# Kernel optimization log

Measured on AMD Instinct MI355X. Metric: run time of the kernel, lower is better.

The kernel has to match this reference:

```python
import jax, jax.numpy as jnp
import numpy as np

OBS = 128; N_AGENT = 16; N_ACTION = 8; N_LAYER = 2; HID = 128
GE = 256; LE = 256; F1 = 512; F2 = 512


def _edges(batch_size, n):
    # all ordered pairs (i, j), i != j, within each sample; GCNConv adds self-loops
    i, j = np.meshgrid(np.arange(n), np.arange(n), indexing='ij')
    m = i != j
    src0, dst0 = i[m], j[m]                      # [n*(n-1)]
    off = (np.arange(batch_size) * n)[:, None]
    src = (src0[None, :] + off).reshape(-1)
    dst = (dst0[None, :] + off).reshape(-1)
    return jnp.asarray(src, jnp.int32), jnp.asarray(dst, jnp.int32)


def setup_inputs() -> dict:
    key = jax.random.key(0)
    ks = jax.random.split(key, 16)
    g = lambda k, shp, fan: jax.random.normal(k, shp, jnp.float32) / np.sqrt(fan)
    return {
        'obs_j': jax.random.normal(ks[0], (2048, N_AGENT, OBS), jnp.float32),
        'W_pre': g(ks[1], (OBS, HID), OBS), 'b_pre': jnp.zeros((HID,), jnp.float32),
        'W_gcn': g(ks[2], (N_LAYER, HID, HID), HID), 'b_gcn': jnp.zeros((N_LAYER, HID), jnp.float32),
        'W_post': g(ks[3], (HID, GE), HID), 'b_post': jnp.zeros((GE,), jnp.float32),
        'W_loc': g(ks[4], (OBS, LE), OBS), 'b_loc': jnp.zeros((LE,), jnp.float32),
        'W1': g(ks[5], (GE + LE, F1), GE + LE), 'b1': jnp.zeros((F1,), jnp.float32),
        'W2': g(ks[6], (F1, F2), F1), 'b2': jnp.zeros((F2,), jnp.float32),
        'W3': g(ks[7], (F2, N_ACTION), F2), 'b3': jnp.zeros((N_ACTION,), jnp.float32),
    }


def reference(obs_j, W_pre, b_pre, W_gcn, b_gcn, W_post, b_post,
              W_loc, b_loc, W1, b1, W2, b2, W3, b3):
    B, n, _ = obs_j.shape
    N = B * n
    obs = obs_j.reshape(N, OBS)
    x = jax.nn.relu(obs @ W_pre + b_pre)          # [N, HID]

    src, dst = _edges(B, n)
    # GCNConv with self-loops on a fully-connected graph: deg = n for every node,
    # edge norm = 1/sqrt(deg_i*deg_j) = 1/n for every (A+I) edge.
    inv_n = jnp.float32(1.0) / n
    for l in range(N_LAYER):
        h = x @ W_gcn[l]                          # lin (no bias inside propagate)
        agg = jax.ops.segment_sum(h[src], dst, num_segments=N)  # neighbor gather/scatter
        x = jax.nn.relu((agg + h) * inv_n + b_gcn[l])            # + self-loop msg, bias

    g = x.reshape(B, n, HID).mean(axis=1)         # global_mean_pool over each graph
    g = jax.nn.relu(g @ W_post + b_post)          # [B, GE]
    loc = jax.nn.relu(obs @ W_loc + b_loc)        # [B*n, LE]
    gi = jnp.repeat(g, n, axis=0)                 # repeat_interleave over agents
    z = jnp.concatenate([gi, loc], axis=1)
    z = jax.nn.relu(z @ W1 + b1)
    z = jax.nn.relu(z @ W2 + b2)
    q = z @ W3 + b3
    return q.reshape(B, n, N_ACTION)
```

## Files before the change

kernel.cpp:

```cpp
#include <hip/hip_runtime.h>
#include <hip/hip_bf16.h>
#include <stdint.h>

typedef __bf16 bf16;
typedef __bf16 bf16x4 __attribute__((ext_vector_type(4)));
typedef __bf16 bf16x8 __attribute__((ext_vector_type(8)));
typedef float f32x4 __attribute__((ext_vector_type(4)));

#define BM 128
#define BN 128
#define BK 64

#define GL(p) ((const __attribute__((address_space(1))) void*)(p))
#define SH(p) ((__attribute__((address_space(3))) void*)(p))

__device__ inline void tp(const float* W, bf16* WT, int id, int shiftK, int N) {
  int K = 1 << shiftK;
  int n = id >> shiftK;
  int k = id & (K - 1);
  WT[id] = (bf16)W[(size_t)k * N + n];
}

__global__ __launch_bounds__(256) void prep_all(
    const float* __restrict__ W1, const float* __restrict__ W2,
    bf16* __restrict__ W1T, bf16* __restrict__ W2T,
    const float* __restrict__ Wpre, const float* __restrict__ Wloc,
    const float* __restrict__ Wgcn, const float* __restrict__ Wpost,
    bf16* __restrict__ WpreLocT, bf16* __restrict__ Wg0T, bf16* __restrict__ Wg1T,
    bf16* __restrict__ WpostT,
    const float* __restrict__ bpre, const float* __restrict__ bloc,
    float* __restrict__ biasPL, float* __restrict__ outq) {
  __shared__ bf16 tile[64 * 68];
  int blk = blockIdx.x;
  int tid = threadIdx.x;
  if (blk < 128) {
    const float* W = (blk < 64) ? W1 : W2;
    bf16* WT = (blk < 64) ? W1T : W2T;
    int t = blk & 63;
    int tk0 = (t >> 3) * 64, tn0 = (t & 7) * 64;
#pragma unroll
    for (int p = 0; p < 4; p++) {
      int kr = p * 16 + (tid >> 4), nc = (tid & 15) * 4;
      float4 f = *(const float4*)(W + (size_t)(tk0 + kr) * 512 + tn0 + nc);
      bf16x4 v; v[0] = (bf16)f.x; v[1] = (bf16)f.y; v[2] = (bf16)f.z; v[3] = (bf16)f.w;
      *(bf16x4*)&tile[kr * 68 + nc] = v;
    }
    __syncthreads();
#pragma unroll
    for (int p = 0; p < 4; p++) {
      int nr = p * 16 + (tid >> 4), kc = (tid & 15) * 4;
      bf16x4 v;
#pragma unroll
      for (int i = 0; i < 4; i++) v[i] = tile[(kc + i) * 68 + nr];
      *(bf16x4*)(WT + (size_t)(tn0 + nr) * 512 + tk0 + kc) = v;
    }
    return;
  }
  blk -= 128;
  if (blk < 448) {
    int id = blk * 256 + tid;
    if (id < 16384) { tp(Wpre, WpreLocT, id, 7, 128); return; } id -= 16384;
    if (id < 32768) { tp(Wloc, WpreLocT + 16384, id, 7, 256); return; } id -= 32768;
    if (id < 16384) { tp(Wgcn, Wg0T, id, 7, 128); return; } id -= 16384;
    if (id < 16384) { tp(Wgcn + 16384, Wg1T, id, 7, 128); return; } id -= 16384;
    tp(Wpost, WpostT, id, 7, 256);
    return;
  }
  blk -= 448;
  if (blk == 0) {
    if (tid < 128) biasPL[tid] = bpre[tid];
    biasPL[128 + tid] = bloc[tid];
    return;
  }
  blk -= 1;
  float4 z = {0.f, 0.f, 0.f, 0.f};
#pragma unroll
  for (int i = 0; i < 4; i++)
    ((float4*)outq)[(size_t)blk * 1024 + i * 256 + tid] = z;
}

template <int NT, int ASRC, bool POOL, bool QFUSE>
__global__ __launch_bounds__(256, 4) void gemm_k(
    const float* __restrict__ Af, const bf16* __restrict__ Ab, const bf16* __restrict__ Ag,
    const bf16* __restrict__ BT, const float* __restrict__ bias,
    bf16* __restrict__ C, int ldc, bf16* __restrict__ pool_out,
    const float* __restrict__ W3, const float* __restrict__ b3, float* __restrict__ outq,
    int M, int K) {
  __shared__ bf16 smem[16384];
  bf16* As = smem;
  bf16* Bs = smem + 8192;

  const int tid = threadIdx.x;
  const int id = blockIdx.x;
  const int s = id >> 3;
  const int n_idx = s % NT;
  const int m0 = ((id & 7) + 8 * (s / NT)) * BM;
  const int n0 = n_idx * BN;

  f32x4 acc[4][4] = {};

  const int lane = tid & 63;
  const int wave = tid >> 6;
  const int wm = (wave >> 1) * 64;
  const int wn = (wave & 1) * 64;
  const int lm = lane & 15;
  const int quad = lane >> 4;

  for (int k0 = 0; k0 < K; k0 += BK) {
#pragma unroll
    for (int it = 0; it < 4; it++) {
      int idx = it * 256 + tid;
      int row = idx >> 3;
      int c = idx & 7;
      int cv8 = c ^ (row & 7);
      int kk = k0 + cv8 * 8;
      if (ASRC == 1) {
        const float* src = Af + (size_t)(m0 + row) * K + kk;
        float4 f0 = *(const float4*)src;
        float4 f1 = *(const float4*)(src + 4);
        bf16x8 v;
        v[0] = (bf16)f0.x; v[1] = (bf16)f0.y; v[2] = (bf16)f0.z; v[3] = (bf16)f0.w;
        v[4] = (bf16)f1.x; v[5] = (bf16)f1.y; v[6] = (bf16)f1.z; v[7] = (bf16)f1.w;
        *(bf16x8*)&As[row * 64 + c * 8] = v;
      } else {
        const bf16* ga;
        if (ASRC == 2) {
          int r = m0 + row;
          ga = (k0 < 256) ? (Ag + (size_t)(r >> 4) * 256 + kk)
                          : (Ab + (size_t)r * 256 + (kk - 256));
        } else {
          ga = Ab + (size_t)(m0 + row) * K + kk;
        }
        __builtin_amdgcn_global_load_lds(GL(ga), SH(&As[(idx & ~63) * 8]), 16, 0, 0);
      }
      const bf16* gb = BT + (size_t)(n0 + row) * K + kk;
      __builtin_amdgcn_global_load_lds(GL(gb), SH(&Bs[(idx & ~63) * 8]), 16, 0, 0);
    }
    __syncthreads();

#pragma unroll
    for (int ks = 0; ks < 2; ks++) {
      const int ua = quad + ks * 4;
      bf16x8 a[4], b[4];
#pragma unroll
      for (int i = 0; i < 4; i++) {
        int r = wm + lm + i * 16;
        a[i] = *(const bf16x8*)&As[r * 64 + ((ua ^ (r & 7)) * 8)];
      }
#pragma unroll
      for (int j = 0; j < 4; j++) {
        int r = wn + lm + j * 16;
        b[j] = *(const bf16x8*)&Bs[r * 64 + ((ua ^ (r & 7)) * 8)];
      }
#pragma unroll
      for (int i = 0; i < 4; i++)
#pragma unroll
        for (int j = 0; j < 4; j++)
          acc[i][j] = __builtin_amdgcn_mfma_f32_16x16x32_bf16(a[i], b[j], acc[i][j], 0, 0, 0);
    }
    __syncthreads();
  }

  if (POOL && n_idx == 0) {
#pragma unroll
    for (int i = 0; i < 4; i++) {
      int sample = (m0 + wm + i * 16) >> 4;
#pragma unroll
      for (int j = 0; j < 4; j++) {
        int col = wn + j * 16 + lm;
        float b = bias[col];
        float v = 0.f;
#pragma unroll
        for (int r = 0; r < 4; r++) v += fmaxf(acc[i][j][r] + b, 0.f);
        v += __shfl_xor(v, 16);
        v += __shfl_xor(v, 32);
        if (quad == 0) pool_out[(size_t)sample * 128 + col] = (bf16)(v * 0.0625f);
      }
    }
  } else if (QFUSE) {
#pragma unroll
    for (int i = 0; i < 4; i++)
#pragma unroll
      for (int j = 0; j < 4; j++) {
        int col = wn + j * 16 + lm;
        float b = bias[n0 + col];
#pragma unroll
        for (int r = 0; r < 4; r++) {
          int row = wm + i * 16 + quad * 4 + r;
          smem[row * 128 + col] = (bf16)fmaxf(acc[i][j][r] + b, 0.f);
        }
      }
    __syncthreads();
    int n = lane & 7;
    int kg = lane >> 3;
    float w3r[16];
#pragma unroll
    for (int i = 0; i < 16; i++) w3r[i] = W3[(size_t)(n0 + kg * 16 + i) * 8 + n];
    float bn = (n_idx == 0) ? b3[n] : 0.f;
    int rbase = wave * 32;
    for (int rr = 0; rr < 32; rr++) {
      const bf16* zr = &smem[(rbase + rr) * 128 + kg * 16];
      bf16x8 z0 = *(const bf16x8*)zr;
      bf16x8 z1v = *(const bf16x8*)(zr + 8);
      float v = 0.f;
#pragma unroll
      for (int i = 0; i < 8; i++) v += (float)z0[i] * w3r[i];
#pragma unroll
      for (int i = 0; i < 8; i++) v += (float)z1v[i] * w3r[8 + i];
      v += __shfl_down(v, 32);
      v += __shfl_down(v, 16);
      v += __shfl_down(v, 8);
      if (lane < 8) atomicAdd(&outq[(size_t)(m0 + rbase + rr) * 8 + n], v + bn);
    }
  } else {
#pragma unroll
    for (int i = 0; i < 4; i++)
#pragma unroll
      for (int j = 0; j < 4; j++) {
        int col = wn + j * 16 + lm;
        float b = bias[n0 + col];
#pragma unroll
        for (int r = 0; r < 4; r++) {
          int row = wm + i * 16 + quad * 4 + r;
          smem[row * 128 + col] = (bf16)fmaxf(acc[i][j][r] + b, 0.f);
        }
      }
    __syncthreads();
    const int coff = POOL ? (n0 - 128) : n0;
#pragma unroll
    for (int c = 0; c < 8; c++) {
      int ci = c * 256 + tid;
      int row = ci >> 4, col8 = (ci & 15) * 8;
      *(bf16x8*)&C[(size_t)(m0 + row) * ldc + coff + col8] = *(const bf16x8*)&smem[row * 128 + col8];
    }
  }
}

__global__ __launch_bounds__(256) void gcn_chain(
    const bf16* __restrict__ xbar, const bf16* __restrict__ Wg0T,
    const bf16* __restrict__ Wg1T, const bf16* __restrict__ WpostT,
    const float* __restrict__ b_gcn, const float* __restrict__ b_post,
    bf16* __restrict__ g) {
  __shared__ bf16 xs[16 * 136];
  __shared__ bf16 ws[256 * 136];
  const int tid = threadIdx.x;
  const int lane = tid & 63, wave = tid >> 6;
  const int lm = lane & 15, quad = lane >> 4;
  const int rb = blockIdx.x * 16;

  {
    int row = tid >> 4, cv = (tid & 15) * 8;
    *(bf16x8*)&xs[row * 136 + cv] = *(const bf16x8*)&xbar[(size_t)(rb + row) * 128 + cv];
  }

  const bf16* Wl[3] = {Wg0T, Wg1T, WpostT};
  const float* bl[3] = {b_gcn, b_gcn + 128, b_post};
  const int Nl[3] = {128, 128, 256};

  for (int l = 0; l < 3; l++) {
    const int N = Nl[l];
    __syncthreads();
    for (int c = tid; c < N * 16; c += 256) {
      int row = c >> 4, cv = (c & 15) * 8;
      *(bf16x8*)&ws[row * 136 + cv] = *(const bf16x8*)&Wl[l][(size_t)row * 128 + cv];
    }
    __syncthreads();
    const int nj = N / 64;
    f32x4 acc[4] = {};
#pragma unroll
    for (int kk = 0; kk < 128; kk += 32) {
      bf16x8 a = *(const bf16x8*)&xs[lm * 136 + quad * 8 + kk];
      for (int j = 0; j < nj; j++) {
        int col = (wave * nj + j) * 16 + lm;
        bf16x8 b = *(const bf16x8*)&ws[col * 136 + quad * 8 + kk];
        acc[j] = __builtin_amdgcn_mfma_f32_16x16x32_bf16(a, b, acc[j], 0, 0, 0);
      }
    }
    __syncthreads();
    const float* bias = bl[l];
    if (l < 2) {
      for (int j = 0; j < nj; j++) {
        int col = (wave * nj + j) * 16 + lm;
        float bv = bias[col];
#pragma unroll
        for (int r = 0; r < 4; r++)
          xs[(quad * 4 + r) * 136 + col] = (bf16)fmaxf(acc[j][r] + bv, 0.f);
      }
    } else {
      for (int j = 0; j < nj; j++) {
        int col = (wave * nj + j) * 16 + lm;
        float bv = bias[col];
#pragma unroll
        for (int r = 0; r < 4; r++)
          g[(size_t)(rb + quad * 4 + r) * 256 + col] = (bf16)fmaxf(acc[j][r] + bv, 0.f);
      }
    }
  }
}

extern "C" void kernel_launch(void* const* d_in, const int* in_sizes, int n_in,
                              void* d_out, int out_size, void* d_ws, size_t ws_size,
                              hipStream_t stream) {
  const float* obs    = (const float*)d_in[0];
  const float* W_pre  = (const float*)d_in[1];
  const float* b_pre  = (const float*)d_in[2];
  const float* W_gcn  = (const float*)d_in[3];
  const float* b_gcn  = (const float*)d_in[4];
  const float* W_post = (const float*)d_in[5];
  const float* b_post = (const float*)d_in[6];
  const float* W_loc  = (const float*)d_in[7];
  const float* b_loc  = (const float*)d_in[8];
  const float* W1     = (const float*)d_in[9];
  const float* b1     = (const float*)d_in[10];
  const float* W2     = (const float*)d_in[11];
  const float* b2     = (const float*)d_in[12];
  const float* W3     = (const float*)d_in[13];
  const float* b3     = (const float*)d_in[14];
  float* out = (float*)d_out;

  char* p = (char*)d_ws;
  auto alloc = [&](size_t bytes) { char* r = p; p += (bytes + 255) & ~(size_t)255; return r; };
  bf16* WpreLocT = (bf16*)alloc(384 * 128 * 2);
  float* biasPL  = (float*)alloc(384 * 4);
  bf16* Wg0T   = (bf16*)alloc(128 * 128 * 2);
  bf16* Wg1T   = (bf16*)alloc(128 * 128 * 2);
  bf16* WpostT = (bf16*)alloc(256 * 128 * 2);
  bf16* W1T    = (bf16*)alloc(512 * 512 * 2);
  bf16* W2T    = (bf16*)alloc(512 * 512 * 2);
  bf16* xbar   = (bf16*)alloc(2048 * 128 * 2);
  bf16* loc    = (bf16*)alloc((size_t)32768 * 256 * 2);
  bf16* g      = (bf16*)alloc(2048 * 256 * 2);
  bf16* z1     = (bf16*)alloc((size_t)32768 * 512 * 2);

  prep_all<<<641, 256, 0, stream>>>(W1, W2, W1T, W2T,
                                    W_pre, W_loc, W_gcn, W_post,
                                    WpreLocT, Wg0T, Wg1T, WpostT,
                                    b_pre, b_loc, biasPL, out);
  gemm_k<3, 1, true, false><<<768, 256, 0, stream>>>(
      obs, nullptr, nullptr, WpreLocT, biasPL, loc, 256, xbar,
      nullptr, nullptr, nullptr, 32768, 128);
  gcn_chain<<<128, 256, 0, stream>>>(xbar, Wg0T, Wg1T, WpostT, b_gcn, b_post, g);
  gemm_k<4, 2, false, false><<<1024, 256, 0, stream>>>(
      nullptr, loc, g, W1T, b1, z1, 512, nullptr,
      nullptr, nullptr, nullptr, 32768, 512);
  gemm_k<4, 0, false, true><<<1024, 256, 0, stream>>>(
      nullptr, z1, nullptr, W2T, b2, nullptr, 0, nullptr,
      W3, b3, out, 32768, 512);
}
```

Before: 174.3 us.

## Fuse all GEMM stages and GCN chain into a single per-row-block megakernel

Replaces the four separate GEMM/GCN launches with one kernel where each block owns 64 rows (4 samples) and runs pre/loc projection, pooling, GCN layers, post, W1, W2 and the W3 reduction in sequence. The q output is accumulated in registers and written directly, which removes the atomics and the zero-init of the output. B operands are now read straight from global memory without LDS staging. loc and z1 still round-trip through global memory within the block. Only 512 blocks with small 64-row tiles may reduce weight reuse and MFMA efficiency.

Measured after the change: 279.1 us. 60.2% more time.

```diff
diff --git a/kernel.cpp b/kernel.cpp
--- a/kernel.cpp
+++ b/kernel.cpp
@@ -7,12 +7,7 @@
 typedef __bf16 bf16x8 __attribute__((ext_vector_type(8)));
 typedef float f32x4 __attribute__((ext_vector_type(4)));
 
-#define BM 128
-#define BN 128
-#define BK 64
-
-#define GL(p) ((const __attribute__((address_space(1))) void*)(p))
-#define SH(p) ((__attribute__((address_space(3))) void*)(p))
+#define MFMA(a, b, c) __builtin_amdgcn_mfma_f32_16x16x32_bf16(a, b, c, 0, 0, 0)
 
 __device__ inline void tp(const float* W, bf16* WT, int id, int shiftK, int N) {
   int K = 1 << shiftK;
@@ -27,9 +22,7 @@
     const float* __restrict__ Wpre, const float* __restrict__ Wloc,
     const float* __restrict__ Wgcn, const float* __restrict__ Wpost,
     bf16* __restrict__ WpreLocT, bf16* __restrict__ Wg0T, bf16* __restrict__ Wg1T,
-    bf16* __restrict__ WpostT,
-    const float* __restrict__ bpre, const float* __restrict__ bloc,
-    float* __restrict__ biasPL, float* __restrict__ outq) {
+    bf16* __restrict__ WpostT) {
   __shared__ bf16 tile[64 * 68];
   int blk = blockIdx.x;
   int tid = threadIdx.x;
@@ -57,244 +50,280 @@
     return;
   }
   blk -= 128;
-  if (blk < 448) {
-    int id = blk * 256 + tid;
-    if (id < 16384) { tp(Wpre, WpreLocT, id, 7, 128); return; } id -= 16384;
-    if (id < 32768) { tp(Wloc, WpreLocT + 16384, id, 7, 256); return; } id -= 32768;
-    if (id < 16384) { tp(Wgcn, Wg0T, id, 7, 128); return; } id -= 16384;
-    if (id < 16384) { tp(Wgcn + 16384, Wg1T, id, 7, 128); return; } id -= 16384;
-    tp(Wpost, WpostT, id, 7, 256);
-    return;
-  }
-  blk -= 448;
-  if (blk == 0) {
-    if (tid < 128) biasPL[tid] = bpre[tid];
-    biasPL[128 + tid] = bloc[tid];
-    return;
-  }
-  blk -= 1;
-  float4 z = {0.f, 0.f, 0.f, 0.f};
-#pragma unroll
-  for (int i = 0; i < 4; i++)
-    ((float4*)outq)[(size_t)blk * 1024 + i * 256 + tid] = z;
+  int id = blk * 256 + tid;
+  if (id < 16384) { tp(Wpre, WpreLocT, id, 7, 128); return; } id -= 16384;
+  if (id < 32768) { tp(Wloc, WpreLocT + 16384, id, 7, 256); return; } id -= 32768;
+  if (id < 16384) { tp(Wgcn, Wg0T, id, 7, 128); return; } id -= 16384;
+  if (id < 16384) { tp(Wgcn + 16384, Wg1T, id, 7, 128); return; } id -= 16384;
+  tp(Wpost, WpostT, id, 7, 256);
 }
 
-template <int NT, int ASRC, bool POOL, bool QFUSE>
-__global__ __launch_bounds__(256, 4) void gemm_k(
-    const float* __restrict__ Af, const bf16* __restrict__ Ab, const bf16* __restrict__ Ag,
-    const bf16* __restrict__ BT, const float* __restrict__ bias,
-    bf16* __restrict__ C, int ldc, bf16* __restrict__ pool_out,
-    const float* __restrict__ W3, const float* __restrict__ b3, float* __restrict__ outq,
-    int M, int K) {
-  __shared__ bf16 smem[16384];
-  bf16* As = smem;
-  bf16* Bs = smem + 8192;
+__global__ __launch_bounds__(256, 2) void mega(
+    const float* __restrict__ obs,
+    const bf16* __restrict__ WpreLocT, const float* __restrict__ b_pre,
+    const float* __restrict__ b_loc,
+    const bf16* __restrict__ Wg0T, const bf16* __restrict__ Wg1T,
+    const bf16* __restrict__ WpostT, const float* __restrict__ b_gcn,
+    const float* __restrict__ b_post,
+    const bf16* __restrict__ W1T, const float* __restrict__ b1,
+    const bf16* __restrict__ W2T, const float* __restrict__ b2,
+    const float* __restrict__ W3, const float* __restrict__ b3,
+    bf16* __restrict__ loc, bf16* __restrict__ z1, float* __restrict__ out) {
+  __shared__ bf16 R0[64 * 136];
+  __shared__ bf16 xbS[16 * 136];
+  __shared__ bf16 x2S[16 * 136];
+  __shared__ bf16 gS[16 * 256];
 
   const int tid = threadIdx.x;
-  const int id = blockIdx.x;
-  const int s = id >> 3;
-  const int n_idx = s % NT;
-  const int m0 = ((id & 7) + 8 * (s / NT)) * BM;
-  const int n0 = n_idx * BN;
-
-  f32x4 acc[4][4] = {};
-
-  const int lane = tid & 63;
-  const int wave = tid >> 6;
-  const int wm = (wave >> 1) * 64;
-  const int wn = (wave & 1) * 64;
-  const int lm = lane & 15;
-  const int quad = lane >> 4;
-
-  for (int k0 = 0; k0 < K; k0 += BK) {
-#pragma unroll
-    for (int it = 0; it < 4; it++) {
-      int idx = it * 256 + tid;
-      int row = idx >> 3;
-      int c = idx & 7;
-      int cv8 = c ^ (row & 7);
-      int kk = k0 + cv8 * 8;
-      if (ASRC == 1) {
-        const float* src = Af + (size_t)(m0 + row) * K + kk;
-        float4 f0 = *(const float4*)src;
-        float4 f1 = *(const float4*)(src + 4);
-        bf16x8 v;
-        v[0] = (bf16)f0.x; v[1] = (bf16)f0.y; v[2] = (bf16)f0.z; v[3] = (bf16)f0.w;
-        v[4] = (bf16)f1.x; v[5] = (bf16)f1.y; v[6] = (bf16)f1.z; v[7] = (bf16)f1.w;
-        *(bf16x8*)&As[row * 64 + c * 8] = v;
-      } else {
-        const bf16* ga;
-        if (ASRC == 2) {
-          int r = m0 + row;
-          ga = (k0 < 256) ? (Ag + (size_t)(r >> 4) * 256 + kk)
-                          : (Ab + (size_t)r * 256 + (kk - 256));
-        } else {
-          ga = Ab + (size_t)(m0 + row) * K + kk;
+  const int lane = tid & 63, wave = tid >> 6;
+  const int wm = (wave >> 1) * 32, wn = (wave & 1) * 64;
+  const int lm = lane & 15, quad = lane >> 4;
+  const int r0 = blockIdx.x * 64;
+
+#pragma unroll
+  for (int it = 0; it < 4; ++it) {
+    int idx = it * 256 + tid;
+    int row = idx >> 4, c = idx & 15;
+    const float* s = obs + (size_t)(r0 + row) * 128 + c * 8;
+    float4 f0 = *(const float4*)s, f1 = *(const float4*)(s + 4);
+    bf16x8 v;
+    v[0] = (bf16)f0.x; v[1] = (bf16)f0.y; v[2] = (bf16)f0.z; v[3] = (bf16)f0.w;
+    v[4] = (bf16)f1.x; v[5] = (bf16)f1.y; v[6] = (bf16)f1.z; v[7] = (bf16)f1.w;
+    *(bf16x8*)&R0[row * 136 + c * 8] = v;
+  }
+  if (tid < 192) {
+    bf16x8 z = {};
+    *(bf16x8*)&xbS[(4 + (tid >> 4)) * 136 + (tid & 15) * 8] = z;
+  }
+  __syncthreads();
+
+  for (int nt = 0; nt < 3; ++nt) {
+    f32x4 acc[2][4] = {};
+#pragma unroll
+    for (int ku = 0; ku < 4; ++ku) {
+      bf16x8 a[2], b[4];
+#pragma unroll
+      for (int i = 0; i < 2; ++i)
+        a[i] = *(const bf16x8*)&R0[(wm + lm + i * 16) * 136 + (ku * 4 + quad) * 8];
+#pragma unroll
+      for (int j = 0; j < 4; ++j)
+        b[j] = *(const bf16x8*)&WpreLocT[(size_t)(nt * 128 + wn + j * 16 + lm) * 128 + ku * 32 + quad * 8];
+#pragma unroll
+      for (int i = 0; i < 2; ++i)
+#pragma unroll
+        for (int j = 0; j < 4; ++j)
+          acc[i][j] = MFMA(a[i], b[j], acc[i][j]);
+    }
+    if (nt == 0) {
+#pragma unroll
+      for (int i = 0; i < 2; ++i) {
+        int sl = (wave >> 1) * 2 + i;
+#pragma unroll
+        for (int j = 0; j < 4; ++j) {
+          int col = wn + j * 16 + lm;
+          float bb = b_pre[col];
+          float v = 0.f;
+#pragma unroll
+          for (int r = 0; r < 4; ++r) v += fmaxf(acc[i][j][r] + bb, 0.f);
+          v += __shfl_xor(v, 16);
+          v += __shfl_xor(v, 32);
+          if (quad == 0) xbS[sl * 136 + col] = (bf16)(v * 0.0625f);
         }
-        __builtin_amdgcn_global_load_lds(GL(ga), SH(&As[(idx & ~63) * 8]), 16, 0, 0);
-      }
-      const bf16* gb = BT + (size_t)(n0 + row) * K + kk;
-      __builtin_amdgcn_global_load_lds(GL(gb), SH(&Bs[(idx & ~63) * 8]), 16, 0, 0);
-    }
-    __syncthreads();
-
-#pragma unroll
-    for (int ks = 0; ks < 2; ks++) {
-      const int ua = quad + ks * 4;
-      bf16x8 a[4], b[4];
-#pragma unroll
-      for (int i = 0; i < 4; i++) {
-        int r = wm + lm + i * 16;
-        a[i] = *(const bf16x8*)&As[r * 64 + ((ua ^ (r & 7)) * 8)];
-      }
-#pragma unroll
-      for (int j = 0; j < 4; j++) {
-        int r = wn + lm + j * 16;
-        b[j] = *(const bf16x8*)&Bs[r * 64 + ((ua ^ (r & 7)) * 8)];
-      }
-#pragma unroll
-      for (int i = 0; i < 4; i++)
-#pragma unroll
-        for (int j = 0; j < 4; j++)
-          acc[i][j] = __builtin_amdgcn_mfma_f32_16x16x32_bf16(a[i], b[j], acc[i][j], 0, 0, 0);
-    }
-    __syncthreads();
-  }
-
-  if (POOL && n_idx == 0) {
-#pragma unroll
-    for (int i = 0; i < 4; i++) {
-      int sample = (m0 + wm + i * 16) >> 4;
-#pragma unroll
-      for (int j = 0; j < 4; j++) {
+      }
+    } else {
+#pragma unroll
+      for (int i = 0; i < 2; ++i)
+#pragma unroll
+        for (int j = 0; j < 4; ++j) {
+          int col = wn + j * 16 + lm;
+          float bb = b_loc[(nt - 1) * 128 + col];
+#pragma unroll
+          for (int r = 0; r < 4; ++r) {
+            int row = r0 + wm + i * 16 + quad * 4 + r;
+            loc[(size_t)row * 256 + (nt - 1) * 128 + col] = (bf16)fmaxf(acc[i][j][r] + bb, 0.f);
+          }
+        }
+    }
+  }
+  __syncthreads();
+
+  {
+    f32x4 a2[2] = {};
+#pragma unroll
+    for (int ku = 0; ku < 4; ++ku) {
+      bf16x8 a = *(const bf16x8*)&xbS[lm * 136 + (ku * 4 + quad) * 8];
+#pragma unroll
+      for (int jn = 0; jn < 2; ++jn) {
+        int col = (wave * 2 + jn) * 16 + lm;
+        bf16x8 b = *(const bf16x8*)&Wg0T[(size_t)col * 128 + ku * 32 + quad * 8];
+        a2[jn] = MFMA(a, b, a2[jn]);
+      }
+    }
+    __syncthreads();
+#pragma unroll
+    for (int jn = 0; jn < 2; ++jn) {
+      int col = (wave * 2 + jn) * 16 + lm;
+      float bb = b_gcn[col];
+#pragma unroll
+      for (int r = 0; r < 4; ++r)
+        x2S[(quad * 4 + r) * 136 + col] = (bf16)fmaxf(a2[jn][r] + bb, 0.f);
+    }
+  }
+  __syncthreads();
+  {
+    f32x4 a2[2] = {};
+#pragma unroll
+    for (int ku = 0; ku < 4; ++ku) {
+      bf16x8 a = *(const bf16x8*)&x2S[lm * 136 + (ku * 4 + quad) * 8];
+#pragma unroll
+      for (int jn = 0; jn < 2; ++jn) {
+        int col = (wave * 2 + jn) * 16 + lm;
+        bf16x8 b = *(const bf16x8*)&Wg1T[(size_t)col * 128 + ku * 32 + quad * 8];
+        a2[jn] = MFMA(a, b, a2[jn]);
+      }
+    }
+    __syncthreads();
+#pragma unroll
+    for (int jn = 0; jn < 2; ++jn) {
+      int col = (wave * 2 + jn) * 16 + lm;
+      float bb = b_gcn[128 + col];
+#pragma unroll
+      for (int r = 0; r < 4; ++r)
+        xbS[(quad * 4 + r) * 136 + col] = (bf16)fmaxf(a2[jn][r] + bb, 0.f);
+    }
+  }
+  __syncthreads();
+  {
+    f32x4 a3[4] = {};
+#pragma unroll
+    for (int ku = 0; ku < 4; ++ku) {
+      bf16x8 a = *(const bf16x8*)&xbS[lm * 136 + (ku * 4 + quad) * 8];
+#pragma unroll
+      for (int jn = 0; jn < 4; ++jn) {
+        int col = (wave * 4 + jn) * 16 + lm;
+        bf16x8 b = *(const bf16x8*)&WpostT[(size_t)col * 128 + ku * 32 + quad * 8];
+        a3[jn] = MFMA(a, b, a3[jn]);
+      }
+    }
+    __syncthreads();
+#pragma unroll
+    for (int jn = 0; jn < 4; ++jn) {
+      int col = (wave * 4 + jn) * 16 + lm;
+      float bb = b_post[col];
+#pragma unroll
+      for (int r = 0; r < 4; ++r)
+        gS[(quad * 4 + r) * 256 + col] = (bf16)fmaxf(a3[jn][r] + bb, 0.f);
+    }
+  }
+  __syncthreads();
+
+  for (int jj = 0; jj < 4; ++jj) {
+    f32x4 acc[2][4] = {};
+#pragma unroll 4
+    for (int ku = 0; ku < 8; ++ku) {
+      bf16x8 a[2], b[4];
+#pragma unroll
+      for (int i = 0; i < 2; ++i) {
+        int sl = (wave >> 1) * 2 + i;
+        a[i] = *(const bf16x8*)&gS[sl * 256 + ku * 32 + quad * 8];
+      }
+#pragma unroll
+      for (int j = 0; j < 4; ++j)
+        b[j] = *(const bf16x8*)&W1T[(size_t)(jj * 128 + wn + j * 16 + lm) * 512 + ku * 32 + quad * 8];
+#pragma unroll
+      for (int i = 0; i < 2; ++i)
+#pragma unroll
+        for (int j = 0; j < 4; ++j)
+          acc[i][j] = MFMA(a[i], b[j], acc[i][j]);
+    }
+#pragma unroll 4
+    for (int ku = 8; ku < 16; ++ku) {
+      bf16x8 a[2], b[4];
+#pragma unroll
+      for (int i = 0; i < 2; ++i)
+        a[i] = *(const bf16x8*)&loc[(size_t)(r0 + wm + lm + i * 16) * 256 + (ku - 8) * 32 + quad * 8];
+#pragma unroll
+      for (int j = 0; j < 4; ++j)
+        b[j] = *(const bf16x8*)&W1T[(size_t)(jj * 128 + wn + j * 16 + lm) * 512 + ku * 32 + quad * 8];
+#pragma unroll
+      for (int i = 0; i < 2; ++i)
+#pragma unroll
+        for (int j = 0; j < 4; ++j)
+          acc[i][j] = MFMA(a[i], b[j], acc[i][j]);
+    }
+#pragma unroll
+    for (int i = 0; i < 2; ++i)
+#pragma unroll
+      for (int j = 0; j < 4; ++j) {
+        int col = jj * 128 + wn + j * 16 + lm;
+        float bb = b1[col];
+#pragma unroll
+        for (int r = 0; r < 4; ++r) {
+          int row = r0 + wm + i * 16 + quad * 4 + r;
+          z1[(size_t)row * 512 + col] = (bf16)fmaxf(acc[i][j][r] + bb, 0.f);
+        }
+      }
+  }
+  __syncthreads();
+
+  float qacc[16];
+#pragma unroll
+  for (int rr = 0; rr < 16; ++rr) qacc[rr] = 0.f;
+  const int qn = lane & 7, kg = lane >> 3;
+
+  for (int jj = 0; jj < 4; ++jj) {
+    f32x4 acc[2][4] = {};
+#pragma unroll 4
+    for (int ku = 0; ku < 16; ++ku) {
+      bf16x8 a[2], b[4];
+#pragma unroll
+      for (int i = 0; i < 2; ++i)
+        a[i] = *(const bf16x8*)&z1[(size_t)(r0 + wm + lm + i * 16) * 512 + ku * 32 + quad * 8];
+#pragma unroll
+      for (int j = 0; j < 4; ++j)
+        b[j] = *(const bf16x8*)&W2T[(size_t)(jj * 128 + wn + j * 16 + lm) * 512 + ku * 32 + quad * 8];
+#pragma unroll
+      for (int i = 0; i < 2; ++i)
+#pragma unroll
+        for (int j = 0; j < 4; ++j)
+          acc[i][j] = MFMA(a[i], b[j], acc[i][j]);
+    }
+    __syncthreads();
+#pragma unroll
+    for (int i = 0; i < 2; ++i)
+#pragma unroll
+      for (int j = 0; j < 4; ++j) {
         int col = wn + j * 16 + lm;
-        float b = bias[col];
-        float v = 0.f;
-#pragma unroll
-        for (int r = 0; r < 4; r++) v += fmaxf(acc[i][j][r] + b, 0.f);
-        v += __shfl_xor(v, 16);
-        v += __shfl_xor(v, 32);
-        if (quad == 0) pool_out[(size_t)sample * 128 + col] = (bf16)(v * 0.0625f);
-      }
-    }
-  } else if (QFUSE) {
-#pragma unroll
-    for (int i = 0; i < 4; i++)
-#pragma unroll
-      for (int j = 0; j < 4; j++) {
-        int col = wn + j * 16 + lm;
-        float b = bias[n0 + col];
-#pragma unroll
-        for (int r = 0; r < 4; r++) {
+        float bb = b2[jj * 128 + col];
+#pragma unroll
+        for (int r = 0; r < 4; ++r) {
           int row = wm + i * 16 + quad * 4 + r;
-          smem[row * 128 + col] = (bf16)fmaxf(acc[i][j][r] + b, 0.f);
+          R0[row * 136 + col] = (bf16)fmaxf(acc[i][j][r] + bb, 0.f);
         }
       }
     __syncthreads();
-    int n = lane & 7;
-    int kg = lane >> 3;
     float w3r[16];
 #pragma unroll
-    for (int i = 0; i < 16; i++) w3r[i] = W3[(size_t)(n0 + kg * 16 + i) * 8 + n];
-    float bn = (n_idx == 0) ? b3[n] : 0.f;
-    int rbase = wave * 32;
-    for (int rr = 0; rr < 32; rr++) {
-      const bf16* zr = &smem[(rbase + rr) * 128 + kg * 16];
-      bf16x8 z0 = *(const bf16x8*)zr;
-      bf16x8 z1v = *(const bf16x8*)(zr + 8);
+    for (int i = 0; i < 16; ++i) w3r[i] = W3[(size_t)(jj * 128 + kg * 16 + i) * 8 + qn];
+    for (int rr = 0; rr < 16; ++rr) {
+      const bf16* zr = &R0[(wave * 16 + rr) * 136 + kg * 16];
+      bf16x8 z0 = *(const bf16x8*)zr, z1v = *(const bf16x8*)(zr + 8);
       float v = 0.f;
 #pragma unroll
-      for (int i = 0; i < 8; i++) v += (float)z0[i] * w3r[i];
-#pragma unroll
-      for (int i = 0; i < 8; i++) v += (float)z1v[i] * w3r[8 + i];
+      for (int i = 0; i < 8; ++i) v += (float)z0[i] * w3r[i];
+#pragma unroll
+      for (int i = 0; i < 8; ++i) v += (float)z1v[i] * w3r[8 + i];
       v += __shfl_down(v, 32);
       v += __shfl_down(v, 16);
       v += __shfl_down(v, 8);
-      if (lane < 8) atomicAdd(&outq[(size_t)(m0 + rbase + rr) * 8 + n], v + bn);
-    }
-  } else {
-#pragma unroll
-    for (int i = 0; i < 4; i++)
-#pragma unroll
-      for (int j = 0; j < 4; j++) {
-        int col = wn + j * 16 + lm;
-        float b = bias[n0 + col];
-#pragma unroll
-        for (int r = 0; r < 4; r++) {
-          int row = wm + i * 16 + quad * 4 + r;
-          smem[row * 128 + col] = (bf16)fmaxf(acc[i][j][r] + b, 0.f);
-        }
-      }
-    __syncthreads();
-    const int coff = POOL ? (n0 - 128) : n0;
-#pragma unroll
-    for (int c = 0; c < 8; c++) {
-      int ci = c * 256 + tid;
-      int row = ci >> 4, col8 = (ci & 15) * 8;
-      *(bf16x8*)&C[(size_t)(m0 + row) * ldc + coff + col8] = *(const bf16x8*)&smem[row * 128 + col8];
-    }
-  }
-}
-
-__global__ __launch_bounds__(256) void gcn_chain(
-    const bf16* __restrict__ xbar, const bf16* __restrict__ Wg0T,
-    const bf16* __restrict__ Wg1T, const bf16* __restrict__ WpostT,
-    const float* __restrict__ b_gcn, const float* __restrict__ b_post,
-    bf16* __restrict__ g) {
-  __shared__ bf16 xs[16 * 136];
-  __shared__ bf16 ws[256 * 136];
-  const int tid = threadIdx.x;
-  const int lane = tid & 63, wave = tid >> 6;
-  const int lm = lane & 15, quad = lane >> 4;
-  const int rb = blockIdx.x * 16;
-
-  {
-    int row = tid >> 4, cv = (tid & 15) * 8;
-    *(bf16x8*)&xs[row * 136 + cv] = *(const bf16x8*)&xbar[(size_t)(rb + row) * 128 + cv];
-  }
-
-  const bf16* Wl[3] = {Wg0T, Wg1T, WpostT};
-  const float* bl[3] = {b_gcn, b_gcn + 128, b_post};
-  const int Nl[3] = {128, 128, 256};
-
-  for (int l = 0; l < 3; l++) {
-    const int N = Nl[l];
-    __syncthreads();
-    for (int c = tid; c < N * 16; c += 256) {
-      int row = c >> 4, cv = (c & 15) * 8;
-      *(bf16x8*)&ws[row * 136 + cv] = *(const bf16x8*)&Wl[l][(size_t)row * 128 + cv];
-    }
-    __syncthreads();
-    const int nj = N / 64;
-    f32x4 acc[4] = {};
-#pragma unroll
-    for (int kk = 0; kk < 128; kk += 32) {
-      bf16x8 a = *(const bf16x8*)&xs[lm * 136 + quad * 8 + kk];
-      for (int j = 0; j < nj; j++) {
-        int col = (wave * nj + j) * 16 + lm;
-        bf16x8 b = *(const bf16x8*)&ws[col * 136 + quad * 8 + kk];
-        acc[j] = __builtin_amdgcn_mfma_f32_16x16x32_bf16(a, b, acc[j], 0, 0, 0);
-      }
-    }
-    __syncthreads();
-    const float* bias = bl[l];
-    if (l < 2) {
-      for (int j = 0; j < nj; j++) {
-        int col = (wave * nj + j) * 16 + lm;
-        float bv = bias[col];
-#pragma unroll
-        for (int r = 0; r < 4; r++)
-          xs[(quad * 4 + r) * 136 + col] = (bf16)fmaxf(acc[j][r] + bv, 0.f);
-      }
-    } else {
-      for (int j = 0; j < nj; j++) {
-        int col = (wave * nj + j) * 16 + lm;
-        float bv = bias[col];
-#pragma unroll
-        for (int r = 0; r < 4; r++)
-          g[(size_t)(rb + quad * 4 + r) * 256 + col] = (bf16)fmaxf(acc[j][r] + bv, 0.f);
-      }
-    }
+      qacc[rr] += v;
+    }
+  }
+  if (lane < 8) {
+    float bb = b3[qn];
+#pragma unroll
+    for (int rr = 0; rr < 16; ++rr)
+      out[(size_t)(r0 + wave * 16 + rr) * 8 + qn] = qacc[rr] + bb;
   }
 }
 
@@ -321,29 +350,19 @@
   char* p = (char*)d_ws;
   auto alloc = [&](size_t bytes) { char* r = p; p += (bytes + 255) & ~(size_t)255; return r; };
   bf16* WpreLocT = (bf16*)alloc(384 * 128 * 2);
-  float* biasPL  = (float*)alloc(384 * 4);
   bf16* Wg0T   = (bf16*)alloc(128 * 128 * 2);
   bf16* Wg1T   = (bf16*)alloc(128 * 128 * 2);
   bf16* WpostT = (bf16*)alloc(256 * 128 * 2);
   bf16* W1T    = (bf16*)alloc(512 * 512 * 2);
   bf16* W2T    = (bf16*)alloc(512 * 512 * 2);
-  bf16* xbar   = (bf16*)alloc(2048 * 128 * 2);
-  bf16* loc    = (bf16*)alloc((size_t)32768 * 256 * 2);
-  bf16* g      = (bf16*)alloc(2048 * 256 * 2);
-  bf16* z1     = (bf16*)alloc((size_t)32768 * 512 * 2);
-
-  prep_all<<<641, 256, 0, stream>>>(W1, W2, W1T, W2T,
+  bf16* locB   = (bf16*)alloc((size_t)32768 * 256 * 2);
+  bf16* z1B    = (bf16*)alloc((size_t)32768 * 512 * 2);
+
+  prep_all<<<576, 256, 0, stream>>>(W1, W2, W1T, W2T,
                                     W_pre, W_loc, W_gcn, W_post,
-                                    WpreLocT, Wg0T, Wg1T, WpostT,
-                                    b_pre, b_loc, biasPL, out);
-  gemm_k<3, 1, true, false><<<768, 256, 0, stream>>>(
-      obs, nullptr, nullptr, WpreLocT, biasPL, loc, 256, xbar,
-      nullptr, nullptr, nullptr, 32768, 128);
-  gcn_chain<<<128, 256, 0, stream>>>(xbar, Wg0T, Wg1T, WpostT, b_gcn, b_post, g);
-  gemm_k<4, 2, false, false><<<1024, 256, 0, stream>>>(
-      nullptr, loc, g, W1T, b1, z1, 512, nullptr,
-      nullptr, nullptr, nullptr, 32768, 512);
-  gemm_k<4, 0, false, true><<<1024, 256, 0, stream>>>(
-      nullptr, z1, nullptr, W2T, b2, nullptr, 0, nullptr,
-      W3, b3, out, 32768, 512);
+                                    WpreLocT, Wg0T, Wg1T, WpostT);
+  mega<<<512, 256, 0, stream>>>(obs, WpreLocT, b_pre, b_loc,
+                                Wg0T, Wg1T, WpostT, b_gcn, b_post,
+                                W1T, b1, W2T, b2, W3, b3,
+                                locB, z1B, out);
 }
```
